# Performance work log

Measured on AMD Instinct MI355X. Metric: run time of the kernel, lower is better.

The kernel has to match this reference:

```python
import jax, jax.numpy as jnp
import numpy as np

B, S, D_IN, D_OUT = 4, 2048, 1024, 64
USE_MASK = True

def setup_inputs() -> dict:
    key = jax.random.key(0)
    ks = jax.random.split(key, 6)
    return {
        "inputs_for_keys": jax.random.normal(ks[0], (B, S, D_IN), jnp.float32),
        "inputs_for_values": jax.random.normal(ks[1], (B, S, D_IN), jnp.float32),
        "inputs_for_queries": jax.random.normal(ks[2], (B, S, D_IN), jnp.float32),
        "Weight_Q": jax.random.normal(ks[3], (D_IN, D_OUT), jnp.float32) * 0.02,
        "Weight_K": jax.random.normal(ks[4], (D_IN, D_OUT), jnp.float32) * 0.02,
        "Weight_V": jax.random.normal(ks[5], (D_IN, D_OUT), jnp.float32) * 0.02,
    }

def reference(inputs_for_keys, inputs_for_values, inputs_for_queries, Weight_Q, Weight_K, Weight_V):
    Q = jnp.einsum('bsd,de->bse', inputs_for_queries, Weight_Q)
    K = jnp.einsum('bsd,de->bse', inputs_for_keys, Weight_K)
    V = jnp.einsum('bsd,de->bse', inputs_for_values, Weight_V)
    # scores: [B, S_q, S_k], scaled by sqrt(d_out)
    scores = jnp.einsum('bqe,bke->bqk', Q, K) / np.sqrt(D_OUT).astype(np.float32)
    if USE_MASK:
        # -inf strictly above the diagonal (causal mask), matching
        # transpose(tril(ones*-inf, -1)) in the original.
        q_idx = jnp.arange(S)[:, None]
        k_idx = jnp.arange(S)[None, :]
        scores = jnp.where(k_idx > q_idx, -jnp.inf, scores)
    attn = jax.nn.softmax(scores, axis=-1)
    return jnp.einsum('bqk,bke->bqe', attn, V)
```

## Files before the change

### kernel.cpp

```cpp
#include <hip/hip_runtime.h>
#include <hip/hip_bf16.h>
#include <stdint.h>

typedef __bf16 bf16_t;
typedef __bf16 bf16x8 __attribute__((ext_vector_type(8)));
typedef float f32x4 __attribute__((ext_vector_type(4)));

#define L2E 1.44269504088896340736f

static __device__ __forceinline__ f32x4 mfma16(bf16x8 a, bf16x8 b, f32x4 c) {
  return __builtin_amdgcn_mfma_f32_16x16x32_bf16(a, b, c, 0, 0, 0);
}

static __device__ __forceinline__ void gload_lds16(const void* g, void* l) {
  __builtin_amdgcn_global_load_lds(
      (const __attribute__((address_space(1))) uint32_t*)g,
      (__attribute__((address_space(3))) uint32_t*)l, 16, 0, 0);
}

static __device__ __forceinline__ float bf2f(uint16_t u) {
  union { uint32_t i; float f; } v; v.i = (uint32_t)u << 16; return v.f;
}

__global__ __launch_bounds__(256) void wt_kernel(const float* __restrict__ Wq,
                                                 const float* __restrict__ Wk,
                                                 const float* __restrict__ Wv,
                                                 bf16_t* __restrict__ Wt) {
  int gid = blockIdx.x * 256 + threadIdx.x;
  int proj = gid >> 16;
  int rem = gid & 65535;
  int k = rem >> 6, n = rem & 63;
  const float* W = (proj == 0) ? Wq : (proj == 1) ? Wk : Wv;
  float v = W[rem];
  if (proj == 0) v *= 0.125f;
  Wt[proj * 65536 + n * 1024 + k] = (bf16_t)v;
}

__global__ __launch_bounds__(512) void proj_kernel(
    const float* __restrict__ Xq, const float* __restrict__ Xk, const float* __restrict__ Xv,
    const bf16_t* __restrict__ Wt,
    bf16_t* __restrict__ Qb, bf16_t* __restrict__ Kb, bf16_t* __restrict__ Vt) {
  __shared__ alignas(16) char Xl[8 * 4096];
  __shared__ alignas(16) bf16_t Msm[8][16][64];

  int tid = threadIdx.x;
  int w = tid >> 6, lane = tid & 63;
  int l15 = lane & 15, g = lane >> 4;
  char* myx = Xl + w * 4096;
  int kw = w;

  bf16x8 Wf[4][4];

  auto loadW = [&](int p) {
    const char* wb = (const char*)Wt + (size_t)p * 131072 + (size_t)kw * 256;
#pragma unroll
    for (int ct = 0; ct < 4; ++ct) {
#pragma unroll
      for (int i = 0; i < 4; ++i) {
        int n = i * 4 + (lane >> 4);
        int srcb = ((lane & 15) * 16) ^ ((n & 7) << 4);
        gload_lds16(wb + (size_t)(ct * 16 + n) * 2048 + srcb, myx + i * 1024);
      }
      asm volatile("s_waitcnt vmcnt(0)" ::: "memory");
      __builtin_amdgcn_sched_barrier(0);
#pragma unroll
      for (int s2 = 0; s2 < 4; ++s2)
        Wf[ct][s2] = *(const bf16x8*)(myx + l15 * 256 + ((s2 * 64 + g * 16) ^ ((l15 & 7) << 4)));
      asm volatile("s_waitcnt lgkmcnt(0)" ::: "memory");
      __builtin_amdgcn_sched_barrier(0);
    }
  };

  f32x4 acc[4] = {};
  float4 xA[4], xB[4];

  auto issueX = [&](int t, int sub, float4* xr) {
    int p = t >> 9, lt = t & 511;
    const float* X = (p == 0) ? Xq : (p == 1) ? Xk : Xv;
    const float* base = X + (size_t)lt * 16384 + kw * 128 + sub * 64 + (lane & 15) * 4;
#pragma unroll
    for (int i = 0; i < 4; ++i)
      xr[i] = *(const float4*)(base + ((lane >> 4) + 4 * i) * 1024);
  };

  auto writeX = [&](const float4* xr, int sub) {
    char* buf = myx + sub * 2048;
#pragma unroll
    for (int i = 0; i < 4; ++i) {
      int rw = (lane >> 4) + 4 * i;
      bf16_t t4[4] = {(bf16_t)xr[i].x, (bf16_t)xr[i].y, (bf16_t)xr[i].z, (bf16_t)xr[i].w};
      *(uint2*)(buf + rw * 128 + (((lane & 15) * 8) ^ ((rw & 7) << 4))) = *(const uint2*)t4;
    }
    asm volatile("s_waitcnt lgkmcnt(0)" ::: "memory");
    __builtin_amdgcn_sched_barrier(0);
  };

  auto computeX = [&](int sub) {
    const char* buf = myx + sub * 2048;
#pragma unroll
    for (int ks = 0; ks < 2; ++ks) {
      bf16x8 af = *(const bf16x8*)(buf + l15 * 128 + ((ks * 64 + g * 16) ^ ((l15 & 7) << 4)));
#pragma unroll
      for (int ct = 0; ct < 4; ++ct)
        acc[ct] = mfma16(af, Wf[ct][sub * 2 + ks], acc[ct]);
    }
  };

  int t0 = blockIdx.x * 3;
  int cur_p = t0 >> 9;
  loadW(cur_p);
  issueX(t0, 0, xA);

#pragma unroll 1
  for (int T = 0; T < 3; ++T) {
    int t = t0 + T;
    int p = t >> 9, lt = t & 511;
    if (p != cur_p) { loadW(p); cur_p = p; }
    issueX(t, 1, xB);
    writeX(xA, 0);
    computeX(0);
    if (T < 2) issueX(t + 1, 0, xA);
    writeX(xB, 1);
    computeX(1);

#pragma unroll
    for (int ct = 0; ct < 4; ++ct)
#pragma unroll
      for (int r = 0; r < 4; ++r)
        Msm[w][g * 4 + r][ct * 16 + l15] = (bf16_t)acc[ct][r];
#pragma unroll
    for (int ct = 0; ct < 4; ++ct) acc[ct] = (f32x4){0.f, 0.f, 0.f, 0.f};
    __syncthreads();

    int row = tid >> 5, c0 = (tid & 31) * 2;
    float s0 = 0.f, s1 = 0.f;
#pragma unroll
    for (int w2 = 0; w2 < 8; ++w2) {
      uint32_t u = *(const uint32_t*)&Msm[w2][row][c0];
      s0 += bf2f((uint16_t)u);
      s1 += bf2f((uint16_t)(u >> 16));
    }

    if (p < 2) {
      bf16_t* Ob = (p == 0) ? Qb : Kb;
      bf16_t o2[2] = {(bf16_t)s0, (bf16_t)s1};
      *(uint32_t*)&Ob[(size_t)(lt * 16 + row) * 64 + c0] = *(const uint32_t*)o2;
      __syncthreads();
    } else {
      __syncthreads();
      bf16_t* Vsm = (bf16_t*)&Msm[0][0][0];
      bf16_t o2[2] = {(bf16_t)s0, (bf16_t)s1};
      *(uint32_t*)&Vsm[row * 72 + c0] = *(const uint32_t*)o2;
      __syncthreads();
      if (tid < 128) {
        int d = tid >> 1, h = tid & 1;
        int b = lt >> 7;
        int s_ = (lt & 127) * 16 + h * 8;
        bf16_t tmp[8];
#pragma unroll
        for (int i = 0; i < 8; ++i) tmp[i] = Vsm[(h * 8 + i) * 72 + d];
        *(uint4*)(Vt + ((size_t)(b * 64 + d)) * 2048 + s_) = *(const uint4*)tmp;
      }
      __syncthreads();
    }
  }
}

#define NW 8
__global__ __launch_bounds__(512) void attn_kernel(
    const bf16_t* __restrict__ Qb, const bf16_t* __restrict__ Kb,
    const bf16_t* __restrict__ Vt, float* __restrict__ Out) {
  __shared__ alignas(16) char Psm[NW * 4096];
  __shared__ float accL[NW][32][64];
  __shared__ float mL[NW][32];
  __shared__ float lL[NW][32];

  int b = blockIdx.y;
  int x = blockIdx.x;
  int qt = (b >= 2) ? (63 - x) : x;
  int q0 = qt * 32;
  int tid = threadIdx.x;
  int w = tid >> 6, lane = tid & 63;
  int l15 = lane & 15, g = lane >> 4;
  char* Pw = Psm + w * 4096;

  bf16x8 qf[2][2];
#pragma unroll
  for (int h = 0; h < 2; ++h) {
    size_t qrow = (size_t)(b * 2048 + q0 + h * 16 + l15) * 64;
    qf[h][0] = *(const bf16x8*)(Qb + qrow + g * 8);
    qf[h][1] = *(const bf16x8*)(Qb + qrow + 32 + g * 8);
  }

  float m_run[2][4], l_run[2][4];
  f32x4 acc_o[2][4] = {};
#pragma unroll
  for (int h = 0; h < 2; ++h)
#pragma unroll
    for (int r = 0; r < 4; ++r) { m_run[h][r] = -1e30f; l_run[h][r] = 0.f; }

  int ntiles = (q0 + 95) >> 6;
  const bf16_t* kbase = Kb + (size_t)b * 2048 * 64;
  const bf16_t* vbase = Vt + (size_t)b * 64 * 2048;

  for (int t = w; t < ntiles; t += NW) {
    int kv0 = t * 64;
    f32x4 s[2][4] = {};
#pragma unroll
    for (int ct = 0; ct < 4; ++ct) {
      const bf16_t* kr = kbase + (size_t)(kv0 + ct * 16 + l15) * 64 + g * 8;
      bf16x8 kf0 = *(const bf16x8*)kr;
      bf16x8 kf1 = *(const bf16x8*)(kr + 32);
#pragma unroll
      for (int h = 0; h < 2; ++h) {
        s[h][ct] = mfma16(qf[h][0], kf0, s[h][ct]);
        s[h][ct] = mfma16(qf[h][1], kf1, s[h][ct]);
      }
    }
    if (t == ntiles - 1) {
#pragma unroll
      for (int h = 0; h < 2; ++h)
#pragma unroll
        for (int ct = 0; ct < 4; ++ct)
#pragma unroll
          for (int r = 0; r < 4; ++r) {
            int kg_ = kv0 + ct * 16 + l15;
            int qg_ = q0 + h * 16 + g * 4 + r;
            if (kg_ > qg_) s[h][ct][r] = -1e30f;
          }
    }

#pragma unroll
    for (int h = 0; h < 2; ++h)
#pragma unroll
      for (int r = 0; r < 4; ++r) {
        float mx = fmaxf(fmaxf(s[h][0][r], s[h][1][r]), fmaxf(s[h][2][r], s[h][3][r]));
        mx = fmaxf(mx, __shfl_xor(mx, 1, 64));
        mx = fmaxf(mx, __shfl_xor(mx, 2, 64));
        mx = fmaxf(mx, __shfl_xor(mx, 4, 64));
        mx = fmaxf(mx, __shfl_xor(mx, 8, 64));
        float mnew = fmaxf(m_run[h][r], mx);
        float scale = exp2f((m_run[h][r] - mnew) * L2E);
        m_run[h][r] = mnew;
        float ps = 0.f;
        int qrl = h * 16 + g * 4 + r;
        char* pb = Pw + qrl * 128;
        int swp = (qrl & 7) << 4;
#pragma unroll
        for (int ct = 0; ct < 4; ++ct) {
          float p = exp2f((s[h][ct][r] - mnew) * L2E);
          ps += p;
          *(bf16_t*)(pb + ((ct * 32 + l15 * 2) ^ swp)) = (bf16_t)p;
        }
        ps += __shfl_xor(ps, 1, 64);
        ps += __shfl_xor(ps, 2, 64);
        ps += __shfl_xor(ps, 4, 64);
        ps += __shfl_xor(ps, 8, 64);
        l_run[h][r] = l_run[h][r] * scale + ps;
#pragma unroll
        for (int dt = 0; dt < 4; ++dt) acc_o[h][dt][r] *= scale;
      }

    int swpr = (l15 & 7) << 4;
#pragma unroll
    for (int ks = 0; ks < 2; ++ks) {
      bf16x8 pf0 = *(const bf16x8*)(Pw + l15 * 128 + ((ks * 64 + g * 16) ^ swpr));
      bf16x8 pf1 = *(const bf16x8*)(Pw + (16 + l15) * 128 + ((ks * 64 + g * 16) ^ swpr));
#pragma unroll
      for (int dt = 0; dt < 4; ++dt) {
        const bf16_t* vr = vbase + (size_t)(dt * 16 + l15) * 2048 + kv0 + ks * 32 + g * 8;
        bf16x8 vf = *(const bf16x8*)vr;
        acc_o[0][dt] = mfma16(pf0, vf, acc_o[0][dt]);
        acc_o[1][dt] = mfma16(pf1, vf, acc_o[1][dt]);
      }
    }
  }

  if (l15 == 0) {
#pragma unroll
    for (int h = 0; h < 2; ++h)
#pragma unroll
      for (int r = 0; r < 4; ++r) {
        mL[w][h * 16 + g * 4 + r] = m_run[h][r];
        lL[w][h * 16 + g * 4 + r] = l_run[h][r];
      }
  }
#pragma unroll
  for (int h = 0; h < 2; ++h)
#pragma unroll
    for (int dt = 0; dt < 4; ++dt)
#pragma unroll
      for (int r = 0; r < 4; ++r)
        accL[w][h * 16 + g * 4 + r][dt * 16 + l15] = acc_o[h][dt][r];
  __syncthreads();

  int row = tid >> 4, c0 = (tid & 15) * 4;
  float M = -1e30f;
#pragma unroll
  for (int w2 = 0; w2 < NW; ++w2) M = fmaxf(M, mL[w2][row]);
  float L = 0.f;
  f32x4 o = {0.f, 0.f, 0.f, 0.f};
#pragma unroll
  for (int w2 = 0; w2 < NW; ++w2) {
    float sc = exp2f((mL[w2][row] - M) * L2E);
    L += lL[w2][row] * sc;
    f32x4 a = *(const f32x4*)&accL[w2][row][c0];
    o[0] += sc * a[0]; o[1] += sc * a[1]; o[2] += sc * a[2]; o[3] += sc * a[3];
  }
  float inv = 1.0f / L;
  float4 o4 = {o[0] * inv, o[1] * inv, o[2] * inv, o[3] * inv};
  *(float4*)&Out[(size_t)(b * 2048 + q0 + row) * 64 + c0] = o4;
}

extern "C" void kernel_launch(void* const* d_in, const int* in_sizes, int n_in,
                              void* d_out, int out_size, void* d_ws, size_t ws_size,
                              hipStream_t stream) {
  const float* Xk = (const float*)d_in[0];
  const float* Xv = (const float*)d_in[1];
  const float* Xq = (const float*)d_in[2];
  const float* Wq = (const float*)d_in[3];
  const float* Wk = (const float*)d_in[4];
  const float* Wv = (const float*)d_in[5];
  float* Out = (float*)d_out;

  bf16_t* ws = (bf16_t*)d_ws;
  bf16_t* Qb = ws;
  bf16_t* Kb = ws + 524288;
  bf16_t* Vt = ws + 1048576;
  bf16_t* Wt = ws + 1572864;

  wt_kernel<<<dim3(768), dim3(256), 0, stream>>>(Wq, Wk, Wv, Wt);
  proj_kernel<<<dim3(512), dim3(512), 0, stream>>>(Xq, Xk, Xv, Wt, Qb, Kb, Vt);
  attn_kernel<<<dim3(64, 4), dim3(512), 0, stream>>>(Qb, Kb, Vt, Out);
}
```

Measured before the change: 52.86 us.

## Restructure projection GEMM to row-tiled blocks with double-buffered weight staging

```diff
diff --git a/kernel.cpp b/kernel.cpp
--- a/kernel.cpp
+++ b/kernel.cpp
@@ -16,10 +16,6 @@
   __builtin_amdgcn_global_load_lds(
       (const __attribute__((address_space(1))) uint32_t*)g,
       (__attribute__((address_space(3))) uint32_t*)l, 16, 0, 0);
-}
-
-static __device__ __forceinline__ float bf2f(uint16_t u) {
-  union { uint32_t i; float f; } v; v.i = (uint32_t)u << 16; return v.f;
 }
 
 __global__ __launch_bounds__(256) void wt_kernel(const float* __restrict__ Wq,
@@ -36,133 +32,101 @@
   Wt[proj * 65536 + n * 1024 + k] = (bf16_t)v;
 }
 
-__global__ __launch_bounds__(512) void proj_kernel(
+__global__ __launch_bounds__(128) void proj_kernel(
     const float* __restrict__ Xq, const float* __restrict__ Xk, const float* __restrict__ Xv,
     const bf16_t* __restrict__ Wt,
     bf16_t* __restrict__ Qb, bf16_t* __restrict__ Kb, bf16_t* __restrict__ Vt) {
-  __shared__ alignas(16) char Xl[8 * 4096];
-  __shared__ alignas(16) bf16_t Msm[8][16][64];
+  __shared__ alignas(16) char Wl[2][16384];
+  __shared__ bf16_t Vb[2][16][68];
 
   int tid = threadIdx.x;
   int w = tid >> 6, lane = tid & 63;
   int l15 = lane & 15, g = lane >> 4;
-  char* myx = Xl + w * 4096;
-  int kw = w;
-
-  bf16x8 Wf[4][4];
-
-  auto loadW = [&](int p) {
-    const char* wb = (const char*)Wt + (size_t)p * 131072 + (size_t)kw * 256;
-#pragma unroll
-    for (int ct = 0; ct < 4; ++ct) {
-#pragma unroll
-      for (int i = 0; i < 4; ++i) {
-        int n = i * 4 + (lane >> 4);
-        int srcb = ((lane & 15) * 16) ^ ((n & 7) << 4);
-        gload_lds16(wb + (size_t)(ct * 16 + n) * 2048 + srcb, myx + i * 1024);
-      }
-      asm volatile("s_waitcnt vmcnt(0)" ::: "memory");
-      __builtin_amdgcn_sched_barrier(0);
-#pragma unroll
-      for (int s2 = 0; s2 < 4; ++s2)
-        Wf[ct][s2] = *(const bf16x8*)(myx + l15 * 256 + ((s2 * 64 + g * 16) ^ ((l15 & 7) << 4)));
-      asm volatile("s_waitcnt lgkmcnt(0)" ::: "memory");
-      __builtin_amdgcn_sched_barrier(0);
+  int bid = blockIdx.x;
+  int p = bid >> 8, rt = bid & 255;
+  int m0 = rt * 32;
+  const float* X = (p == 0) ? Xq : (p == 1) ? Xk : Xv;
+  const char* wbase = (const char*)(Wt + (size_t)p * 65536);
+
+  int sn = w * 4 + (lane >> 4);
+  int skb = (lane & 15) * 16;
+
+  auto stageW = [&](int c, int buf) {
+#pragma unroll
+    for (int i = 0; i < 8; ++i) {
+      int n = i * 8 + sn;
+      const char* src = wbase + (size_t)n * 2048 + c * 256 + (skb ^ ((n & 7) << 4));
+      gload_lds16(src, &Wl[buf][i * 2048 + w * 1024]);
     }
   };
 
+  const float* xrow = X + (size_t)(m0 + w * 16 + l15) * 1024 + g * 8;
+
+  auto issueX = [&](int c, float4* xr) {
+    const float* b = xrow + c * 128;
+#pragma unroll
+    for (int j = 0; j < 4; ++j) {
+      xr[2 * j] = *(const float4*)(b + j * 32);
+      xr[2 * j + 1] = *(const float4*)(b + j * 32 + 4);
+    }
+  };
+
   f32x4 acc[4] = {};
-  float4 xA[4], xB[4];
-
-  auto issueX = [&](int t, int sub, float4* xr) {
-    int p = t >> 9, lt = t & 511;
-    const float* X = (p == 0) ? Xq : (p == 1) ? Xk : Xv;
-    const float* base = X + (size_t)lt * 16384 + kw * 128 + sub * 64 + (lane & 15) * 4;
-#pragma unroll
-    for (int i = 0; i < 4; ++i)
-      xr[i] = *(const float4*)(base + ((lane >> 4) + 4 * i) * 1024);
+
+  auto compute = [&](int c, const float4* xr) {
+    const char* wb = &Wl[c & 1][0];
+#pragma unroll
+    for (int j = 0; j < 4; ++j) {
+      bf16x8 af;
+      af[0] = (bf16_t)xr[2 * j].x; af[1] = (bf16_t)xr[2 * j].y;
+      af[2] = (bf16_t)xr[2 * j].z; af[3] = (bf16_t)xr[2 * j].w;
+      af[4] = (bf16_t)xr[2 * j + 1].x; af[5] = (bf16_t)xr[2 * j + 1].y;
+      af[6] = (bf16_t)xr[2 * j + 1].z; af[7] = (bf16_t)xr[2 * j + 1].w;
+#pragma unroll
+      for (int ct = 0; ct < 4; ++ct) {
+        int n = ct * 16 + l15;
+        bf16x8 bfr = *(const bf16x8*)(wb + n * 256 + ((j * 64 + g * 16) ^ ((n & 7) << 4)));
+        acc[ct] = mfma16(af, bfr, acc[ct]);
+      }
+    }
   };
 
-  auto writeX = [&](const float4* xr, int sub) {
-    char* buf = myx + sub * 2048;
-#pragma unroll
-    for (int i = 0; i < 4; ++i) {
-      int rw = (lane >> 4) + 4 * i;
-      bf16_t t4[4] = {(bf16_t)xr[i].x, (bf16_t)xr[i].y, (bf16_t)xr[i].z, (bf16_t)xr[i].w};
-      *(uint2*)(buf + rw * 128 + (((lane & 15) * 8) ^ ((rw & 7) << 4))) = *(const uint2*)t4;
-    }
-    asm volatile("s_waitcnt lgkmcnt(0)" ::: "memory");
-    __builtin_amdgcn_sched_barrier(0);
-  };
-
-  auto computeX = [&](int sub) {
-    const char* buf = myx + sub * 2048;
-#pragma unroll
-    for (int ks = 0; ks < 2; ++ks) {
-      bf16x8 af = *(const bf16x8*)(buf + l15 * 128 + ((ks * 64 + g * 16) ^ ((l15 & 7) << 4)));
-#pragma unroll
-      for (int ct = 0; ct < 4; ++ct)
-        acc[ct] = mfma16(af, Wf[ct][sub * 2 + ks], acc[ct]);
-    }
-  };
-
-  int t0 = blockIdx.x * 3;
-  int cur_p = t0 >> 9;
-  loadW(cur_p);
-  issueX(t0, 0, xA);
-
-#pragma unroll 1
-  for (int T = 0; T < 3; ++T) {
-    int t = t0 + T;
-    int p = t >> 9, lt = t & 511;
-    if (p != cur_p) { loadW(p); cur_p = p; }
-    issueX(t, 1, xB);
-    writeX(xA, 0);
-    computeX(0);
-    if (T < 2) issueX(t + 1, 0, xA);
-    writeX(xB, 1);
-    computeX(1);
-
+  float4 xA[8], xB[8];
+  stageW(0, 0);
+  issueX(0, xA);
+#pragma unroll
+  for (int c = 0; c < 8; ++c) {
+    __syncthreads();
+    if (c < 7) {
+      stageW(c + 1, (c + 1) & 1);
+      if (c & 1) issueX(c + 1, xA); else issueX(c + 1, xB);
+    }
+    if (c & 1) compute(c, xB); else compute(c, xA);
+  }
+
+  if (p < 2) {
+    bf16_t* Ob = (p == 0) ? Qb : Kb;
+    size_t rbase = (size_t)(m0 + w * 16 + g * 4) * 64 + l15;
 #pragma unroll
     for (int ct = 0; ct < 4; ++ct)
 #pragma unroll
       for (int r = 0; r < 4; ++r)
-        Msm[w][g * 4 + r][ct * 16 + l15] = (bf16_t)acc[ct][r];
-#pragma unroll
-    for (int ct = 0; ct < 4; ++ct) acc[ct] = (f32x4){0.f, 0.f, 0.f, 0.f};
-    __syncthreads();
-
-    int row = tid >> 5, c0 = (tid & 31) * 2;
-    float s0 = 0.f, s1 = 0.f;
-#pragma unroll
-    for (int w2 = 0; w2 < 8; ++w2) {
-      uint32_t u = *(const uint32_t*)&Msm[w2][row][c0];
-      s0 += bf2f((uint16_t)u);
-      s1 += bf2f((uint16_t)(u >> 16));
-    }
-
-    if (p < 2) {
-      bf16_t* Ob = (p == 0) ? Qb : Kb;
-      bf16_t o2[2] = {(bf16_t)s0, (bf16_t)s1};
-      *(uint32_t*)&Ob[(size_t)(lt * 16 + row) * 64 + c0] = *(const uint32_t*)o2;
-      __syncthreads();
-    } else {
-      __syncthreads();
-      bf16_t* Vsm = (bf16_t*)&Msm[0][0][0];
-      bf16_t o2[2] = {(bf16_t)s0, (bf16_t)s1};
-      *(uint32_t*)&Vsm[row * 72 + c0] = *(const uint32_t*)o2;
-      __syncthreads();
-      if (tid < 128) {
-        int d = tid >> 1, h = tid & 1;
-        int b = lt >> 7;
-        int s_ = (lt & 127) * 16 + h * 8;
-        bf16_t tmp[8];
-#pragma unroll
-        for (int i = 0; i < 8; ++i) tmp[i] = Vsm[(h * 8 + i) * 72 + d];
-        *(uint4*)(Vt + ((size_t)(b * 64 + d)) * 2048 + s_) = *(const uint4*)tmp;
-      }
-      __syncthreads();
-    }
+        Ob[rbase + (size_t)r * 64 + ct * 16] = (bf16_t)acc[ct][r];
+  } else {
+#pragma unroll
+    for (int ct = 0; ct < 4; ++ct)
+#pragma unroll
+      for (int r = 0; r < 4; ++r)
+        Vb[w][g * 4 + r][ct * 16 + l15] = (bf16_t)acc[ct][r];
+    int d = lane;
+    bf16_t tmp[16];
+#pragma unroll
+    for (int s = 0; s < 16; ++s) tmp[s] = Vb[w][s][d];
+    int b = rt >> 6;
+    int s0 = (m0 & 2047) + w * 16;
+    bf16_t* dst = Vt + ((size_t)(b * 64 + d)) * 2048 + s0;
+    *(uint4*)dst = *(const uint4*)&tmp[0];
+    *(uint4*)(dst + 8) = *(const uint4*)&tmp[8];
   }
 }
 
@@ -330,6 +294,6 @@
   bf16_t* Wt = ws + 1572864;
 
   wt_kernel<<<dim3(768), dim3(256), 0, stream>>>(Wq, Wk, Wv, Wt);
-  proj_kernel<<<dim3(512), dim3(512), 0, stream>>>(Xq, Xk, Xv, Wt, Qb, Kb, Vt);
+  proj_kernel<<<dim3(768), dim3(128), 0, stream>>>(Xq, Xk, Xv, Wt, Qb, Kb, Vt);
   attn_kernel<<<dim3(64, 4), dim3(512), 0, stream>>>(Qb, Kb, Vt, Out);
 }
```

New measurement: 55.84 us. +5.6%, slower.

## Stage fp32 X tiles via async global-to-LDS loads with double buffering

Applied to the files above, without the earlier changes.

```diff
diff --git a/kernel.cpp b/kernel.cpp
--- a/kernel.cpp
+++ b/kernel.cpp
@@ -20,6 +20,11 @@
 
 static __device__ __forceinline__ float bf2f(uint16_t u) {
   union { uint32_t i; float f; } v; v.i = (uint32_t)u << 16; return v.f;
+}
+
+static __device__ __forceinline__ void lds_barrier() {
+  asm volatile("s_waitcnt lgkmcnt(0)" ::: "memory");
+  __builtin_amdgcn_s_barrier();
 }
 
 __global__ __launch_bounds__(256) void wt_kernel(const float* __restrict__ Wq,
@@ -40,88 +45,90 @@
     const float* __restrict__ Xq, const float* __restrict__ Xk, const float* __restrict__ Xv,
     const bf16_t* __restrict__ Wt,
     bf16_t* __restrict__ Qb, bf16_t* __restrict__ Kb, bf16_t* __restrict__ Vt) {
-  __shared__ alignas(16) char Xl[8 * 4096];
+  __shared__ alignas(16) char Xs[2][65536];
   __shared__ alignas(16) bf16_t Msm[8][16][64];
+  __shared__ bf16_t Vsm[16][68];
 
   int tid = threadIdx.x;
   int w = tid >> 6, lane = tid & 63;
   int l15 = lane & 15, g = lane >> 4;
-  char* myx = Xl + w * 4096;
-  int kw = w;
+  int bid = blockIdx.x;
 
   bf16x8 Wf[4][4];
 
   auto loadW = [&](int p) {
-    const char* wb = (const char*)Wt + (size_t)p * 131072 + (size_t)kw * 256;
-#pragma unroll
-    for (int ct = 0; ct < 4; ++ct) {
-#pragma unroll
-      for (int i = 0; i < 4; ++i) {
-        int n = i * 4 + (lane >> 4);
-        int srcb = ((lane & 15) * 16) ^ ((n & 7) << 4);
-        gload_lds16(wb + (size_t)(ct * 16 + n) * 2048 + srcb, myx + i * 1024);
-      }
-      asm volatile("s_waitcnt vmcnt(0)" ::: "memory");
-      __builtin_amdgcn_sched_barrier(0);
-#pragma unroll
-      for (int s2 = 0; s2 < 4; ++s2)
-        Wf[ct][s2] = *(const bf16x8*)(myx + l15 * 256 + ((s2 * 64 + g * 16) ^ ((l15 & 7) << 4)));
-      asm volatile("s_waitcnt lgkmcnt(0)" ::: "memory");
-      __builtin_amdgcn_sched_barrier(0);
-    }
+    const char* wb = (const char*)Wt + (size_t)p * 131072;
+    char* wreg = &Xs[0][0] + w * 16384;
+#pragma unroll
+    for (int i = 0; i < 16; ++i) {
+      int n = i * 4 + (lane >> 4);
+      const char* src = wb + (size_t)n * 2048 + w * 256 +
+                        (((lane & 15) * 16) ^ ((n & 7) << 4));
+      gload_lds16(src, wreg + i * 1024);
+    }
+    asm volatile("s_waitcnt vmcnt(0)" ::: "memory");
+    __builtin_amdgcn_sched_barrier(0);
+#pragma unroll
+    for (int ct = 0; ct < 4; ++ct)
+#pragma unroll
+      for (int j = 0; j < 4; ++j) {
+        int n = ct * 16 + l15;
+        Wf[ct][j] = *(const bf16x8*)(wreg + n * 256 + ((j * 64 + g * 16) ^ ((n & 7) << 4)));
+      }
   };
 
+  auto stageX = [&](int t_glob, int buf) {
+    int p = t_glob >> 9, t_in = t_glob & 511;
+    const float* X = (p == 0) ? Xq : (p == 1) ? Xk : Xv;
+    const char* xb = (const char*)X + (size_t)t_in * 65536;
+    char* dst = &Xs[buf][0] + w * 8192;
+#pragma unroll
+    for (int i = 0; i < 8; ++i) {
+      int r = w * 2 + (i >> 2), q = i & 3;
+      const char* src = xb + (size_t)r * 4096 + q * 1024 +
+                        ((lane * 16) ^ ((r & 7) << 4));
+      gload_lds16(src, dst + i * 1024);
+    }
+  };
+
   f32x4 acc[4] = {};
-  float4 xA[4], xB[4];
-
-  auto issueX = [&](int t, int sub, float4* xr) {
-    int p = t >> 9, lt = t & 511;
-    const float* X = (p == 0) ? Xq : (p == 1) ? Xk : Xv;
-    const float* base = X + (size_t)lt * 16384 + kw * 128 + sub * 64 + (lane & 15) * 4;
-#pragma unroll
-    for (int i = 0; i < 4; ++i)
-      xr[i] = *(const float4*)(base + ((lane >> 4) + 4 * i) * 1024);
+
+  auto computeX = [&](int buf) {
+    const char* bp = &Xs[buf][0] + l15 * 4096;
+    int swz = (l15 & 7) << 4;
+#pragma unroll
+    for (int j = 0; j < 4; ++j) {
+      int b0 = w * 512 + j * 128 + g * 32;
+      float4 u0 = *(const float4*)(bp + (b0 ^ swz));
+      float4 u1 = *(const float4*)(bp + ((b0 + 16) ^ swz));
+      bf16x8 af;
+      af[0] = (bf16_t)u0.x; af[1] = (bf16_t)u0.y; af[2] = (bf16_t)u0.z; af[3] = (bf16_t)u0.w;
+      af[4] = (bf16_t)u1.x; af[5] = (bf16_t)u1.y; af[6] = (bf16_t)u1.z; af[7] = (bf16_t)u1.w;
+#pragma unroll
+      for (int ct = 0; ct < 4; ++ct)
+        acc[ct] = mfma16(af, Wf[ct][j], acc[ct]);
+    }
   };
 
-  auto writeX = [&](const float4* xr, int sub) {
-    char* buf = myx + sub * 2048;
-#pragma unroll
-    for (int i = 0; i < 4; ++i) {
-      int rw = (lane >> 4) + 4 * i;
-      bf16_t t4[4] = {(bf16_t)xr[i].x, (bf16_t)xr[i].y, (bf16_t)xr[i].z, (bf16_t)xr[i].w};
-      *(uint2*)(buf + rw * 128 + (((lane & 15) * 8) ^ ((rw & 7) << 4))) = *(const uint2*)t4;
-    }
-    asm volatile("s_waitcnt lgkmcnt(0)" ::: "memory");
-    __builtin_amdgcn_sched_barrier(0);
-  };
-
-  auto computeX = [&](int sub) {
-    const char* buf = myx + sub * 2048;
-#pragma unroll
-    for (int ks = 0; ks < 2; ++ks) {
-      bf16x8 af = *(const bf16x8*)(buf + l15 * 128 + ((ks * 64 + g * 16) ^ ((l15 & 7) << 4)));
-#pragma unroll
-      for (int ct = 0; ct < 4; ++ct)
-        acc[ct] = mfma16(af, Wf[ct][sub * 2 + ks], acc[ct]);
-    }
-  };
-
-  int t0 = blockIdx.x * 3;
+  int t0 = bid * 6;
   int cur_p = t0 >> 9;
   loadW(cur_p);
-  issueX(t0, 0, xA);
+  __syncthreads();
+  stageX(t0, 0);
 
 #pragma unroll 1
-  for (int T = 0; T < 3; ++T) {
-    int t = t0 + T;
-    int p = t >> 9, lt = t & 511;
-    if (p != cur_p) { loadW(p); cur_p = p; }
-    issueX(t, 1, xB);
-    writeX(xA, 0);
-    computeX(0);
-    if (T < 2) issueX(t + 1, 0, xA);
-    writeX(xB, 1);
-    computeX(1);
+  for (int i = 0; i < 6; ++i) {
+    int t = t0 + i;
+    int p = t >> 9;
+    if (p != cur_p) {
+      __syncthreads();
+      loadW(p); cur_p = p;
+      __syncthreads();
+      stageX(t, i & 1);
+    }
+    __syncthreads();
+    if (i < 5) stageX(t + 1, (i + 1) & 1);
+    computeX(i & 1);
 
 #pragma unroll
     for (int ct = 0; ct < 4; ++ct)
@@ -130,7 +137,7 @@
         Msm[w][g * 4 + r][ct * 16 + l15] = (bf16_t)acc[ct][r];
 #pragma unroll
     for (int ct = 0; ct < 4; ++ct) acc[ct] = (f32x4){0.f, 0.f, 0.f, 0.f};
-    __syncthreads();
+    lds_barrier();
 
     int row = tid >> 5, c0 = (tid & 31) * 2;
     float s0 = 0.f, s1 = 0.f;
@@ -140,28 +147,24 @@
       s0 += bf2f((uint16_t)u);
       s1 += bf2f((uint16_t)(u >> 16));
     }
-
+    int t_in = t & 511;
     if (p < 2) {
       bf16_t* Ob = (p == 0) ? Qb : Kb;
       bf16_t o2[2] = {(bf16_t)s0, (bf16_t)s1};
-      *(uint32_t*)&Ob[(size_t)(lt * 16 + row) * 64 + c0] = *(const uint32_t*)o2;
-      __syncthreads();
+      *(uint32_t*)&Ob[(size_t)(t_in * 16 + row) * 64 + c0] = *(const uint32_t*)o2;
     } else {
-      __syncthreads();
-      bf16_t* Vsm = (bf16_t*)&Msm[0][0][0];
       bf16_t o2[2] = {(bf16_t)s0, (bf16_t)s1};
-      *(uint32_t*)&Vsm[row * 72 + c0] = *(const uint32_t*)o2;
-      __syncthreads();
+      *(uint32_t*)&Vsm[row][c0] = *(const uint32_t*)o2;
+      lds_barrier();
       if (tid < 128) {
         int d = tid >> 1, h = tid & 1;
-        int b = lt >> 7;
-        int s_ = (lt & 127) * 16 + h * 8;
+        int b = t_in >> 7;
+        int s_ = (t_in & 127) * 16 + h * 8;
         bf16_t tmp[8];
 #pragma unroll
-        for (int i = 0; i < 8; ++i) tmp[i] = Vsm[(h * 8 + i) * 72 + d];
+        for (int s2 = 0; s2 < 8; ++s2) tmp[s2] = Vsm[h * 8 + s2][d];
         *(uint4*)(Vt + ((size_t)(b * 64 + d)) * 2048 + s_) = *(const uint4*)tmp;
       }
-      __syncthreads();
     }
   }
 }
@@ -330,6 +333,6 @@
   bf16_t* Wt = ws + 1572864;
 
   wt_kernel<<<dim3(768), dim3(256), 0, stream>>>(Wq, Wk, Wv, Wt);
-  proj_kernel<<<dim3(512), dim3(512), 0, stream>>>(Xq, Xk, Xv, Wt, Qb, Kb, Vt);
+  proj_kernel<<<dim3(256), dim3(512), 0, stream>>>(Xq, Xk, Xv, Wt, Qb, Kb, Vt);
   attn_kernel<<<dim3(64, 4), dim3(512), 0, stream>>>(Qb, Kb, Vt, Out);
 }
```

Result: no change. 52.85 us (-0.0%).
